# Performance work log

Hardware: AMD Instinct MI355X
Metric: run time of the kernel (lower is better)

The kernel has to match this reference:

```python
import jax, jax.numpy as jnp
import numpy as np

IN_F, OUT_F, GS = 4096, 16384, 128


def setup_inputs() -> dict:
    key = jax.random.key(0)
    k1, k2, k3 = jax.random.split(key, 3)
    x = jax.random.normal(k1, (2, 1024, IN_F), dtype=jnp.float32)
    # ternary codes in {-1, 0, 1}, stored as int8 in the original module
    ternary = jax.random.randint(k2, (OUT_F, IN_F), -1, 2, dtype=jnp.int32)
    n_groups = OUT_F * IN_F // GS
    # per-group scales: positive, like beta = mean(|w|) per group
    scales = jax.random.uniform(k3, (n_groups,), dtype=jnp.float32, minval=0.01, maxval=0.1)
    return {"x": x, "ternary": ternary, "scales": scales}


def reference(x, ternary, scales):
    # Dequantize: each contiguous group of GS flattened weight entries shares one scale.
    w = (ternary.astype(jnp.float32).reshape(-1, GS) * scales[:, None]).reshape(OUT_F, IN_F)
    # F.linear(x, w) == x @ w.T
    return jnp.einsum('bsi,oi->bso', x, w)
```

## Files before the change

kernel.cpp:

```cpp
#include <hip/hip_runtime.h>
#include <stdint.h>

#define M_ROWS 2048
#define IN_F   4096
#define OUT_F  16384

#define BM 256
#define BN 256
#define BK 64
#define NT (IN_F / BK)

typedef __attribute__((ext_vector_type(8))) short short8;
typedef __attribute__((ext_vector_type(4))) float floatx4;

#define FENCE() __asm__ __volatile__("" ::: "memory")
#define BAR()   do { FENCE(); __builtin_amdgcn_s_barrier(); FENCE(); } while (0)

__device__ __forceinline__ unsigned short f32_to_bf16_rne(float f) {
    union { float f; uint32_t u; } v; v.f = f;
    uint32_t u = v.u;
    return (unsigned short)((u + 0x7FFFu + ((u >> 16) & 1u)) >> 16);
}

__global__ __launch_bounds__(256) void convert_x_kernel(
        const float* __restrict__ x, unsigned short* __restrict__ xb) {
    int t = blockIdx.x * 256 + threadIdx.x;
    const float4* p = (const float4*)(x + (size_t)t * 8);
    float4 a = p[0];
    float4 b = p[1];
    short8 o;
    o[0] = (short)f32_to_bf16_rne(a.x);
    o[1] = (short)f32_to_bf16_rne(a.y);
    o[2] = (short)f32_to_bf16_rne(a.z);
    o[3] = (short)f32_to_bf16_rne(a.w);
    o[4] = (short)f32_to_bf16_rne(b.x);
    o[5] = (short)f32_to_bf16_rne(b.y);
    o[6] = (short)f32_to_bf16_rne(b.z);
    o[7] = (short)f32_to_bf16_rne(b.w);
    *(short8*)(xb + (size_t)t * 8) = o;
}

__global__ __launch_bounds__(256) void dequant_w_kernel(
        const int* __restrict__ tern, const float* __restrict__ scales,
        unsigned short* __restrict__ wb) {
    int g = blockIdx.x * 256 + threadIdx.x;
    float s = scales[g >> 4];
    const int4* p = (const int4*)(tern + (size_t)g * 8);
    int4 a = p[0];
    int4 b = p[1];
    short8 o;
    o[0] = (short)f32_to_bf16_rne((float)a.x * s);
    o[1] = (short)f32_to_bf16_rne((float)a.y * s);
    o[2] = (short)f32_to_bf16_rne((float)a.z * s);
    o[3] = (short)f32_to_bf16_rne((float)a.w * s);
    o[4] = (short)f32_to_bf16_rne((float)b.x * s);
    o[5] = (short)f32_to_bf16_rne((float)b.y * s);
    o[6] = (short)f32_to_bf16_rne((float)b.z * s);
    o[7] = (short)f32_to_bf16_rne((float)b.w * s);
    *(short8*)(wb + (size_t)g * 8) = o;
}

__device__ __forceinline__ floatx4 mfma16(short8 a, short8 b, floatx4 c) {
    return __builtin_amdgcn_mfma_f32_16x16x32_bf16(a, b, c, 0, 0, 0);
}

__device__ __forceinline__ void stage_half(
        const unsigned short* G, unsigned short* Ld,
        int row0, int kofs, const int* srow, const int* scol, const int* sub) {
#pragma unroll
    for (int i = 0; i < 2; ++i) {
        const unsigned short* gsrc =
            G + (size_t)(row0 + srow[i]) * IN_F + kofs + scol[i];
        __builtin_amdgcn_global_load_lds(
            (const __attribute__((address_space(1))) void*)gsrc,
            (__attribute__((address_space(3))) void*)(Ld + sub[i]), 16, 0, 0);
    }
}

#define READ_AF(base) \
    _Pragma("unroll") \
    for (int t2 = 0; t2 < 8; ++t2) af[t2] = *(const short8*)((base) + a_off[t2]);

#define MFMA16x2(BF, n0, n1) \
    _Pragma("unroll") \
    for (int t2 = 0; t2 < 8; ++t2) { \
        acc[t2][n0] = mfma16(af[t2], (BF)[0], acc[t2][n0]); \
        acc[t2][n1] = mfma16(af[t2], (BF)[1], acc[t2][n1]); \
    }

__global__ __launch_bounds__(512, 2) void gemm_bt_kernel(
        const unsigned short* __restrict__ A,
        const unsigned short* __restrict__ B,
        float* __restrict__ C) {
    __shared__ unsigned short As[2][2][8192];
    __shared__ unsigned short Bs[2][2][8192];

    const int tid  = threadIdx.x;
    const int lane = tid & 63;
    const int quad = lane >> 4;
    const int frow = lane & 15;
    const int w    = tid >> 6;
    const int wr   = w >> 2;
    const int wc   = w & 3;

    const int bid = blockIdx.x;
    const int swz = (bid & 7) * 64 + (bid >> 3);
    const int bm  = (swz & 7) * BM;
    const int bn  = (swz >> 3) * BN;

    int a_off[8], b_off[4];
#pragma unroll
    for (int t2 = 0; t2 < 8; ++t2) {
        int r = wr * 128 + t2 * 16 + frow;
        a_off[t2] = (r >> 1) * 64 +
                    (((((r & 1) << 2) + quad) ^ ((r >> 1) & 7)) << 3);
    }
#pragma unroll
    for (int nf = 0; nf < 4; ++nf) {
        int r = wc * 64 + nf * 16 + frow;
        b_off[nf] = (r >> 1) * 64 +
                    (((((r & 1) << 2) + quad) ^ ((r >> 1) & 7)) << 3);
    }

    int srow[2], scol[2], sub[2];
#pragma unroll
    for (int i = 0; i < 2; ++i) {
        int cid = i * 512 + tid;
        int ln  = cid >> 3;
        int k8  = (cid & 7) ^ (ln & 7);
        srow[i] = 2 * ln + (k8 >> 2);
        scol[i] = (k8 & 3) * 8;
        sub[i]  = (i * 512 + (tid & 448)) * 8;
    }

    floatx4 acc[8][4] = {};
    short8 af[8], bfA[2], bfB[2];

    stage_half(A, &As[0][0][0], bm, 0,  srow, scol, sub);
    stage_half(B, &Bs[0][0][0], bn, 0,  srow, scol, sub);
    stage_half(A, &As[0][1][0], bm, 32, srow, scol, sub);
    stage_half(B, &Bs[0][1][0], bn, 32, srow, scol, sub);

#pragma unroll 1
    for (int t = 0; t < NT - 1; ++t) {
        const int buf = t & 1, nbuf = buf ^ 1;
        const int ktn = (t + 1) * BK;
        const unsigned short* a0 = &As[buf][0][0];
        const unsigned short* a1 = &As[buf][1][0];
        const unsigned short* b0 = &Bs[buf][0][0];
        const unsigned short* b1 = &Bs[buf][1][0];

        stage_half(A, &As[nbuf][0][0], bm, ktn, srow, scol, sub);
        __asm__ __volatile__("s_waitcnt vmcnt(6)" ::: "memory");
        BAR();
        READ_AF(a0);
        bfA[0] = *(const short8*)(b0 + b_off[0]);
        bfA[1] = *(const short8*)(b0 + b_off[1]);
        __builtin_amdgcn_s_setprio(1);
        MFMA16x2(bfA, 0, 1);
        __builtin_amdgcn_s_setprio(0);

        stage_half(B, &Bs[nbuf][0][0], bn, ktn, srow, scol, sub);
        __asm__ __volatile__("s_waitcnt vmcnt(6)" ::: "memory");
        BAR();
        bfB[0] = *(const short8*)(b0 + b_off[2]);
        bfB[1] = *(const short8*)(b0 + b_off[3]);
        __builtin_amdgcn_s_setprio(1);
        MFMA16x2(bfB, 2, 3);
        __builtin_amdgcn_s_setprio(0);

        stage_half(A, &As[nbuf][1][0], bm, ktn + 32, srow, scol, sub);
        __asm__ __volatile__("s_waitcnt vmcnt(6)" ::: "memory");
        BAR();
        READ_AF(a1);
        bfA[0] = *(const short8*)(b1 + b_off[0]);
        bfA[1] = *(const short8*)(b1 + b_off[1]);
        __builtin_amdgcn_s_setprio(1);
        MFMA16x2(bfA, 0, 1);
        __builtin_amdgcn_s_setprio(0);

        stage_half(B, &Bs[nbuf][1][0], bn, ktn + 32, srow, scol, sub);
        __asm__ __volatile__("s_waitcnt vmcnt(6)" ::: "memory");
        BAR();
        bfB[0] = *(const short8*)(b1 + b_off[2]);
        bfB[1] = *(const short8*)(b1 + b_off[3]);
        __builtin_amdgcn_s_setprio(1);
        MFMA16x2(bfB, 2, 3);
        __builtin_amdgcn_s_setprio(0);
    }

    {
        const unsigned short* a0 = &As[(NT - 1) & 1][0][0];
        const unsigned short* a1 = &As[(NT - 1) & 1][1][0];
        const unsigned short* b0 = &Bs[(NT - 1) & 1][0][0];
        const unsigned short* b1 = &Bs[(NT - 1) & 1][1][0];

        __asm__ __volatile__("s_waitcnt vmcnt(4)" ::: "memory");
        BAR();
        READ_AF(a0);
        bfA[0] = *(const short8*)(b0 + b_off[0]);
        bfA[1] = *(const short8*)(b0 + b_off[1]);
        bfB[0] = *(const short8*)(b0 + b_off[2]);
        bfB[1] = *(const short8*)(b0 + b_off[3]);
        __builtin_amdgcn_s_setprio(1);
        MFMA16x2(bfA, 0, 1);
        MFMA16x2(bfB, 2, 3);
        __builtin_amdgcn_s_setprio(0);

        __asm__ __volatile__("s_waitcnt vmcnt(0)" ::: "memory");
        BAR();
        READ_AF(a1);
        bfA[0] = *(const short8*)(b1 + b_off[0]);
        bfA[1] = *(const short8*)(b1 + b_off[1]);
        bfB[0] = *(const short8*)(b1 + b_off[2]);
        bfB[1] = *(const short8*)(b1 + b_off[3]);
        __builtin_amdgcn_s_setprio(1);
        MFMA16x2(bfA, 0, 1);
        MFMA16x2(bfB, 2, 3);
        __builtin_amdgcn_s_setprio(0);
    }

    const int row0 = bm + wr * 128 + quad * 4;
    const int col0 = bn + wc * 64 + frow;
#pragma unroll
    for (int t2 = 0; t2 < 8; ++t2) {
#pragma unroll
        for (int nf = 0; nf < 4; ++nf) {
            float* cp = C + (size_t)(row0 + t2 * 16) * OUT_F + (col0 + nf * 16);
#pragma unroll
            for (int r = 0; r < 4; ++r)
                cp[(size_t)r * OUT_F] = acc[t2][nf][r];
        }
    }
}

extern "C" void kernel_launch(void* const* d_in, const int* in_sizes, int n_in,
                              void* d_out, int out_size, void* d_ws, size_t ws_size,
                              hipStream_t stream) {
    const float* x     = (const float*)d_in[0];
    const int*   tern  = (const int*)d_in[1];
    const float* scal  = (const float*)d_in[2];
    float*       out   = (float*)d_out;

    unsigned short* xb = (unsigned short*)d_ws;
    unsigned short* wb = xb + (size_t)M_ROWS * IN_F;

    convert_x_kernel<<<(M_ROWS * IN_F / 8) / 256, 256, 0, stream>>>(x, xb);
    dequant_w_kernel<<<((size_t)OUT_F * IN_F / 8) / 256, 256, 0, stream>>>(tern, scal, wb);
    gemm_bt_kernel<<<dim3((M_ROWS / BM) * (OUT_F / BN)), 512, 0, stream>>>(xb, wb, out);
}
```

Before: 714.5 us.

## Switch GEMM mainloop to four-stage K=32 LDS ring with prefetch depth three

Restructures the bf16 GEMM main loop from a double-buffered BK=64 scheme into a 4-slot LDS ring of BK=32 tiles, prefetching three tiles ahead with global_load_lds. Each tile runs as two MFMA halves over the M fragments, with A/B staging interleaved between barriers, and register fragments drop from 8+4 to 4+4. The goal is deeper latency hiding of global loads and lower register pressure. The cost is more barriers per unit of K work and 128KB of LDS per block, which likely limits occupancy below the declared two blocks per CU.

```diff
diff --git a/kernel.cpp b/kernel.cpp
--- a/kernel.cpp
+++ b/kernel.cpp
@@ -7,7 +7,7 @@
 
 #define BM 256
 #define BN 256
-#define BK 64
+#define BK 32
 #define NT (IN_F / BK)
 
 typedef __attribute__((ext_vector_type(8))) short short8;
@@ -15,6 +15,7 @@
 
 #define FENCE() __asm__ __volatile__("" ::: "memory")
 #define BAR()   do { FENCE(); __builtin_amdgcn_s_barrier(); FENCE(); } while (0)
+#define PH_VM(N) __asm__ __volatile__("s_waitcnt vmcnt(" #N ")" ::: "memory")
 
 __device__ __forceinline__ unsigned short f32_to_bf16_rne(float f) {
     union { float f; uint32_t u; } v; v.f = f;
@@ -77,23 +78,51 @@
     }
 }
 
-#define READ_AF(base) \
-    _Pragma("unroll") \
-    for (int t2 = 0; t2 < 8; ++t2) af[t2] = *(const short8*)((base) + a_off[t2]);
-
-#define MFMA16x2(BF, n0, n1) \
-    _Pragma("unroll") \
-    for (int t2 = 0; t2 < 8; ++t2) { \
-        acc[t2][n0] = mfma16(af[t2], (BF)[0], acc[t2][n0]); \
-        acc[t2][n1] = mfma16(af[t2], (BF)[1], acc[t2][n1]); \
-    }
+#define TILE(T, DOSTAGE, VMCODE) do {                                         \
+    const unsigned short* _as = &As[(T) & 3][0];                              \
+    const unsigned short* _bs = &Bs[(T) & 3][0];                              \
+       \
+    _Pragma("unroll")                                                         \
+    for (int _m = 0; _m < 4; ++_m) af[_m] = *(const short8*)(_as + a_off[_m]);\
+    _Pragma("unroll")                                                         \
+    for (int _n = 0; _n < 4; ++_n) bf[_n] = *(const short8*)(_bs + b_off[_n]);\
+    if (DOSTAGE)                                                              \
+        stage_half(A, &As[((T) + 3) & 3][0], bm, ((T) + 3) * BK,              \
+                   srow, scol, sub);                                          \
+    BAR();                                                                    \
+    __builtin_amdgcn_s_setprio(1);                                            \
+    _Pragma("unroll")                                                         \
+    for (int _m = 0; _m < 4; ++_m)                                            \
+        _Pragma("unroll")                                                     \
+        for (int _n = 0; _n < 4; ++_n)                                        \
+            acc[_m][_n] = mfma16(af[_m], bf[_n], acc[_m][_n]);                \
+    __builtin_amdgcn_s_setprio(0);                                            \
+    BAR();                                                                    \
+     \
+    _Pragma("unroll")                                                         \
+    for (int _m = 0; _m < 4; ++_m)                                            \
+        af[_m] = *(const short8*)(_as + a_off[4 + _m]);                       \
+    if (DOSTAGE)                                                              \
+        stage_half(B, &Bs[((T) + 3) & 3][0], bn, ((T) + 3) * BK,              \
+                   srow, scol, sub);                                          \
+    BAR();                                                                    \
+    __builtin_amdgcn_s_setprio(1);                                            \
+    _Pragma("unroll")                                                         \
+    for (int _m = 0; _m < 4; ++_m)                                            \
+        _Pragma("unroll")                                                     \
+        for (int _n = 0; _n < 4; ++_n)                                        \
+            acc[4 + _m][_n] = mfma16(af[_m], bf[_n], acc[4 + _m][_n]);        \
+    __builtin_amdgcn_s_setprio(0);                                            \
+    VMCODE;                                                                   \
+    BAR();                                                                    \
+} while (0)
 
 __global__ __launch_bounds__(512, 2) void gemm_bt_kernel(
         const unsigned short* __restrict__ A,
         const unsigned short* __restrict__ B,
         float* __restrict__ C) {
-    __shared__ unsigned short As[2][2][8192];
-    __shared__ unsigned short Bs[2][2][8192];
+    __shared__ unsigned short As[4][8192];
+    __shared__ unsigned short Bs[4][8192];
 
     const int tid  = threadIdx.x;
     const int lane = tid & 63;
@@ -110,9 +139,9 @@
 
     int a_off[8], b_off[4];
 #pragma unroll
-    for (int t2 = 0; t2 < 8; ++t2) {
-        int r = wr * 128 + t2 * 16 + frow;
-        a_off[t2] = (r >> 1) * 64 +
+    for (int mf = 0; mf < 8; ++mf) {
+        int r = wr * 128 + mf * 16 + frow;
+        a_off[mf] = (r >> 1) * 64 +
                     (((((r & 1) << 2) + quad) ^ ((r >> 1) & 7)) << 3);
     }
 #pragma unroll
@@ -134,102 +163,35 @@
     }
 
     floatx4 acc[8][4] = {};
-    short8 af[8], bfA[2], bfB[2];
-
-    stage_half(A, &As[0][0][0], bm, 0,  srow, scol, sub);
-    stage_half(B, &Bs[0][0][0], bn, 0,  srow, scol, sub);
-    stage_half(A, &As[0][1][0], bm, 32, srow, scol, sub);
-    stage_half(B, &Bs[0][1][0], bn, 32, srow, scol, sub);
+    short8 af[4], bf[4];
+
+    stage_half(A, &As[0][0], bm, 0 * BK, srow, scol, sub);
+    stage_half(B, &Bs[0][0], bn, 0 * BK, srow, scol, sub);
+    stage_half(A, &As[1][0], bm, 1 * BK, srow, scol, sub);
+    stage_half(B, &Bs[1][0], bn, 1 * BK, srow, scol, sub);
+    stage_half(A, &As[2][0], bm, 2 * BK, srow, scol, sub);
+    stage_half(B, &Bs[2][0], bn, 2 * BK, srow, scol, sub);
+    PH_VM(8);
+    BAR();
 
 #pragma unroll 1
-    for (int t = 0; t < NT - 1; ++t) {
-        const int buf = t & 1, nbuf = buf ^ 1;
-        const int ktn = (t + 1) * BK;
-        const unsigned short* a0 = &As[buf][0][0];
-        const unsigned short* a1 = &As[buf][1][0];
-        const unsigned short* b0 = &Bs[buf][0][0];
-        const unsigned short* b1 = &Bs[buf][1][0];
-
-        stage_half(A, &As[nbuf][0][0], bm, ktn, srow, scol, sub);
-        __asm__ __volatile__("s_waitcnt vmcnt(6)" ::: "memory");
-        BAR();
-        READ_AF(a0);
-        bfA[0] = *(const short8*)(b0 + b_off[0]);
-        bfA[1] = *(const short8*)(b0 + b_off[1]);
-        __builtin_amdgcn_s_setprio(1);
-        MFMA16x2(bfA, 0, 1);
-        __builtin_amdgcn_s_setprio(0);
-
-        stage_half(B, &Bs[nbuf][0][0], bn, ktn, srow, scol, sub);
-        __asm__ __volatile__("s_waitcnt vmcnt(6)" ::: "memory");
-        BAR();
-        bfB[0] = *(const short8*)(b0 + b_off[2]);
-        bfB[1] = *(const short8*)(b0 + b_off[3]);
-        __builtin_amdgcn_s_setprio(1);
-        MFMA16x2(bfB, 2, 3);
-        __builtin_amdgcn_s_setprio(0);
-
-        stage_half(A, &As[nbuf][1][0], bm, ktn + 32, srow, scol, sub);
-        __asm__ __volatile__("s_waitcnt vmcnt(6)" ::: "memory");
-        BAR();
-        READ_AF(a1);
-        bfA[0] = *(const short8*)(b1 + b_off[0]);
-        bfA[1] = *(const short8*)(b1 + b_off[1]);
-        __builtin_amdgcn_s_setprio(1);
-        MFMA16x2(bfA, 0, 1);
-        __builtin_amdgcn_s_setprio(0);
-
-        stage_half(B, &Bs[nbuf][1][0], bn, ktn + 32, srow, scol, sub);
-        __asm__ __volatile__("s_waitcnt vmcnt(6)" ::: "memory");
-        BAR();
-        bfB[0] = *(const short8*)(b1 + b_off[2]);
-        bfB[1] = *(const short8*)(b1 + b_off[3]);
-        __builtin_amdgcn_s_setprio(1);
-        MFMA16x2(bfB, 2, 3);
-        __builtin_amdgcn_s_setprio(0);
-    }
-
-    {
-        const unsigned short* a0 = &As[(NT - 1) & 1][0][0];
-        const unsigned short* a1 = &As[(NT - 1) & 1][1][0];
-        const unsigned short* b0 = &Bs[(NT - 1) & 1][0][0];
-        const unsigned short* b1 = &Bs[(NT - 1) & 1][1][0];
-
-        __asm__ __volatile__("s_waitcnt vmcnt(4)" ::: "memory");
-        BAR();
-        READ_AF(a0);
-        bfA[0] = *(const short8*)(b0 + b_off[0]);
-        bfA[1] = *(const short8*)(b0 + b_off[1]);
-        bfB[0] = *(const short8*)(b0 + b_off[2]);
-        bfB[1] = *(const short8*)(b0 + b_off[3]);
-        __builtin_amdgcn_s_setprio(1);
-        MFMA16x2(bfA, 0, 1);
-        MFMA16x2(bfB, 2, 3);
-        __builtin_amdgcn_s_setprio(0);
-
-        __asm__ __volatile__("s_waitcnt vmcnt(0)" ::: "memory");
-        BAR();
-        READ_AF(a1);
-        bfA[0] = *(const short8*)(b1 + b_off[0]);
-        bfA[1] = *(const short8*)(b1 + b_off[1]);
-        bfB[0] = *(const short8*)(b1 + b_off[2]);
-        bfB[1] = *(const short8*)(b1 + b_off[3]);
-        __builtin_amdgcn_s_setprio(1);
-        MFMA16x2(bfA, 0, 1);
-        MFMA16x2(bfB, 2, 3);
-        __builtin_amdgcn_s_setprio(0);
-    }
+    for (int t = 0; t < NT - 3; ++t) {
+        TILE(t, true, PH_VM(8));
+    }
+    TILE(NT - 3, false, PH_VM(4));
+    TILE(NT - 2, false, PH_VM(0));
+    TILE(NT - 1, false, (void)0);
 
     const int row0 = bm + wr * 128 + quad * 4;
     const int col0 = bn + wc * 64 + frow;
 #pragma unroll
-    for (int t2 = 0; t2 < 8; ++t2) {
+    for (int mf = 0; mf < 8; ++mf) {
 #pragma unroll
         for (int nf = 0; nf < 4; ++nf) {
-            float* cp = C + (size_t)(row0 + t2 * 16) * OUT_F + (col0 + nf * 16);
+            float* cp = C + (size_t)(row0 + mf * 16) * OUT_F + (col0 + nf * 16);
 #pragma unroll
             for (int r = 0; r < 4; ++r)
-                cp[(size_t)r * OUT_F] = acc[t2][nf][r];
+                cp[(size_t)r * OUT_F] = acc[mf][nf][r];
         }
     }
 }
```

Result: slower. 752.6 us (+5.3%).
